# Performance work log

Hardware: AMD Instinct MI355X
Metric: run time of the kernel (lower is better)

The kernel has to match this reference:

```python
import jax, jax.numpy as jnp
import numpy as np

D_MODEL, H, D_FF = 1024, 16, 4096
D_K = D_MODEL // H
EPS = 1e-5


def _layernorm(x, alpha, bias):
    # faithful to source: unbiased std (ddof=1), eps added to std (not var)
    mean = jnp.mean(x, axis=-1, keepdims=True)
    std = jnp.std(x, axis=-1, keepdims=True, ddof=1)
    return alpha * (x - mean) / (std + EPS) + bias


def setup_inputs() -> dict:
    key = jax.random.key(0)
    ks = jax.random.split(key, 12)
    B, S = 2, 2048
    s = 1.0 / np.sqrt(D_MODEL)
    inp = {
        "x": jax.random.normal(ks[0], (B, S, D_MODEL), dtype=jnp.float32),
        "mask": jnp.ones((B, 1, 1, S), dtype=jnp.int32),
        "wq": jax.random.normal(ks[1], (D_MODEL, D_MODEL), dtype=jnp.float32) * s,
        "wk": jax.random.normal(ks[2], (D_MODEL, D_MODEL), dtype=jnp.float32) * s,
        "wv": jax.random.normal(ks[3], (D_MODEL, D_MODEL), dtype=jnp.float32) * s,
        "wo": jax.random.normal(ks[4], (D_MODEL, D_MODEL), dtype=jnp.float32) * s,
        "w1": jax.random.normal(ks[5], (D_MODEL, D_FF), dtype=jnp.float32) * s,
        "b1": jnp.zeros((D_FF,), dtype=jnp.float32),
        "w2": jax.random.normal(ks[6], (D_FF, D_MODEL), dtype=jnp.float32) * (1.0 / np.sqrt(D_FF)),
        "b2": jnp.zeros((D_MODEL,), dtype=jnp.float32),
        "alpha1": jnp.ones((1,), dtype=jnp.float32),
        "bias1": jnp.zeros((1,), dtype=jnp.float32),
        "alpha2": jnp.ones((1,), dtype=jnp.float32),
        "bias2": jnp.zeros((1,), dtype=jnp.float32),
    }
    return inp


def reference(x, mask, wq, wk, wv, wo, w1, b1, w2, b2, alpha1, bias1, alpha2, bias2):
    B, S, _ = x.shape

    # --- sublayer 1: pre-norm self-attention + residual ---
    xn = _layernorm(x, alpha1, bias1)
    q = (xn @ wq).reshape(B, S, H, D_K).transpose(0, 2, 1, 3)  # [B,H,S,Dk]
    k = (xn @ wk).reshape(B, S, H, D_K).transpose(0, 2, 1, 3)
    v = (xn @ wv).reshape(B, S, H, D_K).transpose(0, 2, 1, 3)

    scores = jnp.einsum("bhqd,bhkd->bhqk", q, k) / np.sqrt(D_K)  # [B,H,S,S]
    scores = jnp.where(mask == 0, jnp.float32(-1e9), scores)
    attn = jax.nn.softmax(scores, axis=-1)
    ctx = jnp.einsum("bhqk,bhkd->bhqd", attn, v)
    ctx = ctx.transpose(0, 2, 1, 3).reshape(B, S, D_MODEL)
    x = x + ctx @ wo

    # --- sublayer 2: pre-norm FFN + residual ---
    xn = _layernorm(x, alpha2, bias2)
    h = jax.nn.relu(xn @ w1 + b1)
    x = x + h @ w2 + b2
    return x
```

## Files before the change

kernel.cpp:

```cpp
#include <hip/hip_runtime.h>
#include <hip/hip_bf16.h>

typedef __attribute__((ext_vector_type(8))) short bf16x8;
typedef __attribute__((ext_vector_type(4))) short short4v;
typedef __attribute__((ext_vector_type(4))) float floatx4;

#define MFMA16(A, B, C) __builtin_amdgcn_mfma_f32_16x16x32_bf16((A), (B), (C), 0, 0, 0)

__device__ inline short bf16bits(float f) {
  __hip_bfloat16 h = __float2bfloat16(f);
  return *reinterpret_cast<short*>(&h);
}
__device__ inline unsigned cvtpk(float lo, float hi) {
  unsigned r;
  asm("v_cvt_pk_bf16_f32 %0, %1, %2" : "=v"(r) : "v"(lo), "v"(hi));
  return r;
}
typedef __attribute__((address_space(3))) char lds_char;
typedef __attribute__((address_space(1))) const char glob_char;
__device__ inline void gll16(const void* g, void* l) {
  __builtin_amdgcn_global_load_lds((glob_char*)g, (lds_char*)l, 16, 0, 0);
}

__global__ __launch_bounds__(256) void ln_qkvtrans_kernel(
    const float* __restrict__ x, __hip_bfloat16* __restrict__ y,
    const float* __restrict__ alpha_p, const float* __restrict__ bias_p,
    const float* __restrict__ wq, const float* __restrict__ wk,
    const float* __restrict__ wv, __hip_bfloat16* __restrict__ wqkvT) {
  __shared__ __align__(16) __hip_bfloat16 tile[64][72];
  const int bid = blockIdx.x;
  const int t = threadIdx.x;
  if (bid < 4096) {
    __shared__ float sred[8];
    const float* xr = x + (long)bid * 1024;
    float v[4];
#pragma unroll
    for (int i = 0; i < 4; i++) v[i] = xr[t * 4 + i];
    float sum = 0.f, sq = 0.f;
#pragma unroll
    for (int i = 0; i < 4; i++) { sum += v[i]; sq += v[i] * v[i]; }
#pragma unroll
    for (int off = 32; off; off >>= 1) {
      sum += __shfl_down(sum, off);
      sq += __shfl_down(sq, off);
    }
    if ((t & 63) == 0) { sred[(t >> 6) * 2] = sum; sred[(t >> 6) * 2 + 1] = sq; }
    __syncthreads();
    sum = sred[0] + sred[2] + sred[4] + sred[6];
    sq = sred[1] + sred[3] + sred[5] + sred[7];
    const float mean = sum * (1.f / 1024.f);
    float var = (sq - 1024.f * mean * mean) * (1.f / 1023.f);
    var = fmaxf(var, 0.f);
    const float denom = sqrtf(var) + 1e-5f;
    const float sc = alpha_p[0] / denom;
    const float beta = bias_p[0];
    __hip_bfloat16* yr = y + (long)bid * 1024;
#pragma unroll
    for (int i = 0; i < 4; i++) yr[t * 4 + i] = __float2bfloat16((v[i] - mean) * sc + beta);
  } else {
    const int tt = bid - 4096;
    const int which = tt >> 8;
    const float* src = which == 0 ? wq : (which == 1 ? wk : wv);
    __hip_bfloat16* dst = wqkvT + (size_t)which * 1024 * 1024;
    const long r0 = (long)((tt >> 4) & 15) * 64, c0 = (long)(tt & 15) * 64;
    for (int i = t; i < 1024; i += 256) {
      int r = i >> 4, c4 = (i & 15) * 4;
      float4 f = *(const float4*)&src[(r0 + r) * 1024 + c0 + c4];
      short4v s;
      s[0] = bf16bits(f.x); s[1] = bf16bits(f.y);
      s[2] = bf16bits(f.z); s[3] = bf16bits(f.w);
      *(short4v*)&tile[r][c4] = s;
    }
    __syncthreads();
    for (int i = t; i < 512; i += 256) {
      int c = i >> 3, r8 = (i & 7) * 8;
      bf16x8 sv;
#pragma unroll
      for (int j = 0; j < 8; j++) sv[j] = *reinterpret_cast<const short*>(&tile[r8 + j][c]);
      *(bf16x8*)&dst[(c0 + c) * 1024 + r0 + r8] = sv;
    }
  }
}

__global__ __launch_bounds__(256) void prep_kernel(
    const __hip_bfloat16* __restrict__ qkv, __hip_bfloat16* __restrict__ vt,
    const float* __restrict__ wo, __hip_bfloat16* __restrict__ woT,
    const int* __restrict__ mask, float* __restrict__ addm,
    int* __restrict__ flags) {
  __shared__ __align__(16) __hip_bfloat16 tile[64][72];
  __shared__ int ok[4];
  const int bid = blockIdx.x;
  if (bid < 1024) {
    const int bh = bid >> 5, b = bh >> 4, h = bh & 15;
    const long s0 = (long)(bid & 31) * 64;
    const __hip_bfloat16* src = qkv + ((long)b * 2048 + s0) * 3072 + 2048 + h * 64;
    for (int i = threadIdx.x; i < 512; i += 256) {
      int s = i >> 3, d8 = (i & 7) * 8;
      *(uint4*)&tile[s][d8] = *(const uint4*)&src[(long)s * 3072 + d8];
    }
    __syncthreads();
    __hip_bfloat16* dstb = vt + (long)bh * 64 * 2048 + s0;
    for (int i = threadIdx.x; i < 512; i += 256) {
      int d = i >> 3, s8 = (i & 7) * 8;
      bf16x8 sv;
#pragma unroll
      for (int j = 0; j < 8; j++) sv[j] = *reinterpret_cast<const short*>(&tile[s8 + j][d]);
      *(bf16x8*)&dstb[(long)d * 2048 + s8] = sv;
    }
  } else if (bid < 1280) {
    const int t = bid - 1024;
    const long r0 = (long)(t >> 4) * 64, c0 = (long)(t & 15) * 64;
    for (int i = threadIdx.x; i < 1024; i += 256) {
      int r = i >> 4, c4 = (i & 15) * 4;
      float4 f = *(const float4*)&wo[(r0 + r) * 1024 + c0 + c4];
      short4v s;
      s[0] = bf16bits(f.x); s[1] = bf16bits(f.y);
      s[2] = bf16bits(f.z); s[3] = bf16bits(f.w);
      *(short4v*)&tile[r][c4] = s;
    }
    __syncthreads();
    for (int i = threadIdx.x; i < 512; i += 256) {
      int c = i >> 3, r8 = (i & 7) * 8;
      bf16x8 sv;
#pragma unroll
      for (int j = 0; j < 8; j++) sv[j] = *reinterpret_cast<const short*>(&tile[r8 + j][c]);
      *(bf16x8*)&woT[(c0 + c) * 1024 + r0 + r8] = sv;
    }
  } else {
    const int i = (bid - 1280) * 256 + threadIdx.x;
    const int mv = mask[i];
    addm[i] = mv ? 0.f : -1e30f;
    const unsigned long long bal = __ballot(mv != 0);
    if ((threadIdx.x & 63) == 0) ok[threadIdx.x >> 6] = (bal == ~0ull) ? 1 : 0;
    __syncthreads();
    if (threadIdx.x == 0) flags[bid - 1280] = ok[0] & ok[1] & ok[2] & ok[3];
  }
}

__global__ __launch_bounds__(256) void ln2_wtrans_kernel(
    const float* __restrict__ x1, __hip_bfloat16* __restrict__ xn2,
    const float* __restrict__ alpha_p, const float* __restrict__ bias_p,
    const float* __restrict__ w1c, const float* __restrict__ w2c,
    __hip_bfloat16* __restrict__ w1Th, __hip_bfloat16* __restrict__ w2Th) {
  __shared__ __align__(16) __hip_bfloat16 tile[64][72];
  const int bid = blockIdx.x;
  const int t = threadIdx.x;
  if (bid < 4096) {
    __shared__ float sred[8];
    const float* xr = x1 + (long)bid * 1024;
    float v[4];
#pragma unroll
    for (int i = 0; i < 4; i++) v[i] = xr[t * 4 + i];
    float sum = 0.f, sq = 0.f;
#pragma unroll
    for (int i = 0; i < 4; i++) { sum += v[i]; sq += v[i] * v[i]; }
#pragma unroll
    for (int off = 32; off; off >>= 1) {
      sum += __shfl_down(sum, off);
      sq += __shfl_down(sq, off);
    }
    if ((t & 63) == 0) { sred[(t >> 6) * 2] = sum; sred[(t >> 6) * 2 + 1] = sq; }
    __syncthreads();
    sum = sred[0] + sred[2] + sred[4] + sred[6];
    sq = sred[1] + sred[3] + sred[5] + sred[7];
    const float mean = sum * (1.f / 1024.f);
    float var = (sq - 1024.f * mean * mean) * (1.f / 1023.f);
    var = fmaxf(var, 0.f);
    const float denom = sqrtf(var) + 1e-5f;
    const float sc = alpha_p[0] / denom;
    const float beta = bias_p[0];
    __hip_bfloat16* yr = xn2 + (long)bid * 1024;
#pragma unroll
    for (int i = 0; i < 4; i++) yr[t * 4 + i] = __float2bfloat16((v[i] - mean) * sc + beta);
  } else {
    const int wb = bid - 4096;
    const float* src;
    __hip_bfloat16* dst;
    int R, ldS;
    long r0, c0;
    if (wb < 512) {
      src = w1c; dst = w1Th; R = 1024; ldS = 4096;
      r0 = (long)(wb >> 5) * 64; c0 = (long)(wb & 31) * 64;
    } else {
      const int t2 = wb - 512;
      src = w2c; dst = w2Th; R = 2048; ldS = 1024;
      r0 = (long)(t2 >> 4) * 64; c0 = (long)(t2 & 15) * 64;
    }
    for (int i = t; i < 1024; i += 256) {
      int r = i >> 4, c4 = (i & 15) * 4;
      float4 f = *(const float4*)&src[(r0 + r) * ldS + c0 + c4];
      short4v s;
      s[0] = bf16bits(f.x); s[1] = bf16bits(f.y);
      s[2] = bf16bits(f.z); s[3] = bf16bits(f.w);
      *(short4v*)&tile[r][c4] = s;
    }
    __syncthreads();
    for (int i = t; i < 512; i += 256) {
      int c = i >> 3, r8 = (i & 7) * 8;
      bf16x8 sv;
#pragma unroll
      for (int j = 0; j < 8; j++) sv[j] = *reinterpret_cast<const short*>(&tile[r8 + j][c]);
      *(bf16x8*)&dst[(c0 + c) * R + r0 + r8] = sv;
    }
  }
}

__global__ __launch_bounds__(256) void wtrans_kernel(
    const float* __restrict__ w1c, const float* __restrict__ w2c,
    __hip_bfloat16* __restrict__ w1Th, __hip_bfloat16* __restrict__ w2Th) {
  __shared__ __align__(16) __hip_bfloat16 tile[64][72];
  const int bid = blockIdx.x;
  const float* src;
  __hip_bfloat16* dst;
  int R, ldS;
  long r0, c0;
  if (bid < 512) {
    src = w1c; dst = w1Th; R = 1024; ldS = 4096;
    r0 = (long)(bid >> 5) * 64; c0 = (long)(bid & 31) * 64;
  } else {
    const int t = bid - 512;
    src = w2c; dst = w2Th; R = 2048; ldS = 1024;
    r0 = (long)(t >> 4) * 64; c0 = (long)(t & 15) * 64;
  }
  for (int i = threadIdx.x; i < 1024; i += 256) {
    int r = i >> 4, c4 = (i & 15) * 4;
    float4 f = *(const float4*)&src[(r0 + r) * ldS + c0 + c4];
    short4v s;
    s[0] = bf16bits(f.x); s[1] = bf16bits(f.y);
    s[2] = bf16bits(f.z); s[3] = bf16bits(f.w);
    *(short4v*)&tile[r][c4] = s;
  }
  __syncthreads();
  for (int i = threadIdx.x; i < 512; i += 256) {
    int c = i >> 3, r8 = (i & 7) * 8;
    bf16x8 sv;
#pragma unroll
    for (int j = 0; j < 8; j++) sv[j] = *reinterpret_cast<const short*>(&tile[r8 + j][c]);
    *(bf16x8*)&dst[(c0 + c) * R + r0 + r8] = sv;
  }
}

__global__ __launch_bounds__(256) void bias_add_kernel(
    const float* __restrict__ x1, const float* __restrict__ b2,
    float* __restrict__ out) {
  const int i = (blockIdx.x * 256 + threadIdx.x) * 4;
  float4 v = *(const float4*)&x1[i];
  const float4 bb = *(const float4*)&b2[i & 1023];
  v.x += bb.x; v.y += bb.y; v.z += bb.z; v.w += bb.w;
  *(float4*)&out[i] = v;
}

template <int EPI>
__global__ __launch_bounds__(256) void gemm_bt_kernel(
    const __hip_bfloat16* __restrict__ A, const __hip_bfloat16* __restrict__ Bt,
    void* __restrict__ Cv, const float* __restrict__ bias,
    const float* __restrict__ res, int M, int N, int K) {
  __shared__ __align__(16) __hip_bfloat16 lA[2][128 * 32];
  __shared__ __align__(16) __hip_bfloat16 lB[2][128 * 32];
  const int tid = threadIdx.x;
  const int wave = tid >> 6, lane = tid & 63;
  const int quad = lane >> 4, l16 = lane & 15;
  const int wm = wave >> 1, wn = wave & 1;

  const int gx = gridDim.x;
  const int nwg = gx * gridDim.y;
  int bid = blockIdx.y * gx + blockIdx.x;
  bid = (bid & 7) * (nwg >> 3) + (bid >> 3);
  const long m0 = (long)(bid / gx) * 128;
  const long n0 = (long)(bid % gx) * 128;

  const int rA0 = tid >> 2, cA0 = (tid & 3) * 8;
  const int rA1 = (tid + 256) >> 2, cA1 = ((tid + 256) & 3) * 8;

  floatx4 acc[4][4];
#pragma unroll
  for (int i = 0; i < 4; i++)
#pragma unroll
    for (int j = 0; j < 4; j++) acc[i][j] = (floatx4){0.f, 0.f, 0.f, 0.f};

  const __hip_bfloat16* Ab = A + m0 * K;
  const __hip_bfloat16* Bb = Bt + n0 * K;

  gll16(&Ab[(long)rA0 * K + cA0], &lA[0][wave * 512]);
  gll16(&Ab[(long)rA1 * K + cA1], &lA[0][2048 + wave * 512]);
  gll16(&Bb[(long)rA0 * K + cA0], &lB[0][wave * 512]);
  gll16(&Bb[(long)rA1 * K + cA1], &lB[0][2048 + wave * 512]);

  int cur = 0;
  for (int k0 = 0; k0 < K; k0 += 32) {
    __syncthreads();
    if (k0 + 32 < K) {
      const int nxt = cur ^ 1;
      gll16(&Ab[(long)rA0 * K + k0 + 32 + cA0], &lA[nxt][wave * 512]);
      gll16(&Ab[(long)rA1 * K + k0 + 32 + cA1], &lA[nxt][2048 + wave * 512]);
      gll16(&Bb[(long)rA0 * K + k0 + 32 + cA0], &lB[nxt][wave * 512]);
      gll16(&Bb[(long)rA1 * K + k0 + 32 + cA1], &lB[nxt][2048 + wave * 512]);
    }
    bf16x8 af[4], bfr[4];
#pragma unroll
    for (int mi = 0; mi < 4; mi++)
      af[mi] = *(const bf16x8*)&lA[cur][(wm * 64 + mi * 16 + l16) * 32 + quad * 8];
#pragma unroll
    for (int ni = 0; ni < 4; ni++)
      bfr[ni] = *(const bf16x8*)&lB[cur][(wn * 64 + ni * 16 + l16) * 32 + quad * 8];
#pragma unroll
    for (int mi = 0; mi < 4; mi++)
#pragma unroll
      for (int ni = 0; ni < 4; ni++)
        acc[mi][ni] = MFMA16(af[mi], bfr[ni], acc[mi][ni]);
    cur ^= 1;
  }

#pragma unroll
  for (int mi = 0; mi < 4; mi++) {
#pragma unroll
    for (int ni = 0; ni < 4; ni++) {
#pragma unroll
      for (int r = 0; r < 4; r++) {
        const long row = m0 + wm * 64 + mi * 16 + quad * 4 + r;
        const long col = n0 + wn * 64 + ni * 16 + l16;
        const long idx = row * N + col;
        float v = acc[mi][ni][r];
        if (EPI == 0) {
          ((__hip_bfloat16*)Cv)[idx] = __float2bfloat16(v);
        } else if (EPI == 1) {
          ((float*)Cv)[idx] = v + res[idx];
        } else if (EPI == 2) {
          v += bias[col];
          ((__hip_bfloat16*)Cv)[idx] = __float2bfloat16(fmaxf(v, 0.f));
        } else if (EPI == 3) {
          float* Cf = (float*)Cv;
          Cf[idx] = Cf[idx] + v;
        }
      }
    }
  }
}

template <int EPI>
__global__ __launch_bounds__(256) void gemm_bt_k64_kernel(
    const __hip_bfloat16* __restrict__ A, const __hip_bfloat16* __restrict__ Bt,
    void* __restrict__ Cv, const float* __restrict__ bias,
    const float* __restrict__ res, int M, int N, int K) {
  __shared__ __align__(16) __hip_bfloat16 lA[2][128 * 64];
  __shared__ __align__(16) __hip_bfloat16 lB[2][128 * 64];
  const int tid = threadIdx.x;
  const int wave = tid >> 6, lane = tid & 63;
  const int quad = lane >> 4, l16 = lane & 15;
  const int wm = wave >> 1, wn = wave & 1;

  const int gx = gridDim.x;
  const int nwg = gx * gridDim.y;
  int bid = blockIdx.y * gx + blockIdx.x;
  bid = (bid & 7) * (nwg >> 3) + (bid >> 3);
  const long m0 = (long)(bid / gx) * 128;
  const long n0 = (long)(bid % gx) * 128;

  const int srow = lane >> 3;
  const int cg = (lane & 7) ^ srow;

  floatx4 acc[4][4];
#pragma unroll
  for (int i = 0; i < 4; i++)
#pragma unroll
    for (int j = 0; j < 4; j++) acc[i][j] = (floatx4){0.f, 0.f, 0.f, 0.f};

  const __hip_bfloat16* Ab = A + m0 * K;
  const __hip_bfloat16* Bb = Bt + n0 * K;

#pragma unroll
  for (int j = 0; j < 4; ++j) {
    const int c = wave + j * 4;
    gll16(&Ab[(long)(c * 8 + srow) * K + cg * 8], &lA[0][c * 512]);
    gll16(&Bb[(long)(c * 8 + srow) * K + cg * 8], &lB[0][c * 512]);
  }

  int cur = 0;
  for (int k0 = 0; k0 < K; k0 += 64) {
    __syncthreads();
    if (k0 + 64 < K) {
      const int nxt = cur ^ 1;
#pragma unroll
      for (int j = 0; j < 4; ++j) {
        const int c = wave + j * 4;
        gll16(&Ab[(long)(c * 8 + srow) * K + k0 + 64 + cg * 8], &lA[nxt][c * 512]);
        gll16(&Bb[(long)(c * 8 + srow) * K + k0 + 64 + cg * 8], &lB[nxt][c * 512]);
      }
    }
#pragma unroll
    for (int ks = 0; ks < 2; ++ks) {
      bf16x8 af[4], bfr[4];
#pragma unroll
      for (int mi = 0; mi < 4; mi++) {
        const int row = wm * 64 + mi * 16 + l16;
        af[mi] = *(const bf16x8*)&lA[cur][row * 64 +
                                          (((ks * 4 + quad) ^ (l16 & 7)) * 8)];
      }
#pragma unroll
      for (int ni = 0; ni < 4; ni++) {
        const int row = wn * 64 + ni * 16 + l16;
        bfr[ni] = *(const bf16x8*)&lB[cur][row * 64 +
                                           (((ks * 4 + quad) ^ (l16 & 7)) * 8)];
      }
#pragma unroll
      for (int mi = 0; mi < 4; mi++)
#pragma unroll
        for (int ni = 0; ni < 4; ni++)
          acc[mi][ni] = MFMA16(af[mi], bfr[ni], acc[mi][ni]);
    }
    cur ^= 1;
  }

#pragma unroll
  for (int mi = 0; mi < 4; mi++) {
#pragma unroll
    for (int ni = 0; ni < 4; ni++) {
#pragma unroll
      for (int r = 0; r < 4; r++) {
        const long row = m0 + wm * 64 + mi * 16 + quad * 4 + r;
        const long col = n0 + wn * 64 + ni * 16 + l16;
        const long idx = row * N + col;
        float v = acc[mi][ni][r];
        if (EPI == 0) {
          ((__hip_bfloat16*)Cv)[idx] = __float2bfloat16(v);
        } else if (EPI == 1) {
          ((float*)Cv)[idx] = v + res[idx];
        } else if (EPI == 2) {
          v += bias[col];
          ((__hip_bfloat16*)Cv)[idx] = __float2bfloat16(fmaxf(v, 0.f));
        } else if (EPI == 3) {
          float* Cf = (float*)Cv;
          Cf[idx] = Cf[idx] + v;
        }
      }
    }
  }
}

template <int EPI>
__global__ __launch_bounds__(256) void gemm64_bt_kernel(
    const __hip_bfloat16* __restrict__ A, const __hip_bfloat16* __restrict__ Bt,
    void* __restrict__ Cv, const float* __restrict__ bias,
    const float* __restrict__ res, int M, int N, int K) {
  __shared__ __align__(16) __hip_bfloat16 lA[2][128 * 64];
  __shared__ __align__(16) __hip_bfloat16 lB[2][64 * 64];
  const int tid = threadIdx.x;
  const int wave = tid >> 6, lane = tid & 63;
  const int quad = lane >> 4, l16 = lane & 15;
  const int wm = wave >> 1, wn = wave & 1;

  const int gx = gridDim.x;
  const int nwg = gx * gridDim.y;
  int bid = blockIdx.y * gx + blockIdx.x;
  bid = (bid & 7) * (nwg >> 3) + (bid >> 3);
  const long m0 = (long)(bid / gx) * 128;
  const long n0 = (long)(bid % gx) * 64;

  const int srow = lane >> 3;
  const int cg = (lane & 7) ^ srow;

  floatx4 acc[4][2];
#pragma unroll
  for (int i = 0; i < 4; i++)
#pragma unroll
    for (int j = 0; j < 2; j++) acc[i][j] = (floatx4){0.f, 0.f, 0.f, 0.f};

  const __hip_bfloat16* Ab = A + m0 * K;
  const __hip_bfloat16* Bb = Bt + n0 * K;

#pragma unroll
  for (int j = 0; j < 4; ++j) {
    const int c = wave + j * 4;
    gll16(&Ab[(long)(c * 8 + srow) * K + cg * 8], &lA[0][c * 512]);
  }
#pragma unroll
  for (int j = 0; j < 2; ++j) {
    const int c = wave + j * 4;
    gll16(&Bb[(long)(c * 8 + srow) * K + cg * 8], &lB[0][c * 512]);
  }

  int cur = 0;
  for (int k0 = 0; k0 < K; k0 += 64) {
    __syncthreads();
    if (k0 + 64 < K) {
      const int nxt = cur ^ 1;
#pragma unroll
      for (int j = 0; j < 4; ++j) {
        const int c = wave + j * 4;
        gll16(&Ab[(long)(c * 8 + srow) * K + k0 + 64 + cg * 8], &lA[nxt][c * 512]);
      }
#pragma unroll
      for (int j = 0; j < 2; ++j) {
        const int c = wave + j * 4;
        gll16(&Bb[(long)(c * 8 + srow) * K + k0 + 64 + cg * 8], &lB[nxt][c * 512]);
      }
    }
#pragma unroll
    for (int ks = 0; ks < 2; ++ks) {
      bf16x8 af[4], bfr[2];
#pragma unroll
      for (int mi = 0; mi < 4; mi++) {
        const int row = wm * 64 + mi * 16 + l16;
        af[mi] = *(const bf16x8*)&lA[cur][row * 64 +
                                          (((ks * 4 + quad) ^ (l16 & 7)) * 8)];
      }
#pragma unroll
      for (int ni = 0; ni < 2; ni++) {
        const int row = wn * 32 + ni * 16 + l16;
        bfr[ni] = *(const bf16x8*)&lB[cur][row * 64 +
                                           (((ks * 4 + quad) ^ (l16 & 7)) * 8)];
      }
#pragma unroll
      for (int mi = 0; mi < 4; mi++)
#pragma unroll
        for (int ni = 0; ni < 2; ni++)
          acc[mi][ni] = MFMA16(af[mi], bfr[ni], acc[mi][ni]);
    }
    cur ^= 1;
  }

#pragma unroll
  for (int mi = 0; mi < 4; mi++) {
#pragma unroll
    for (int ni = 0; ni < 2; ni++) {
#pragma unroll
      for (int r = 0; r < 4; r++) {
        const long row = m0 + wm * 64 + mi * 16 + quad * 4 + r;
        const long col = n0 + wn * 32 + ni * 16 + l16;
        const long idx = row * N + col;
        float v = acc[mi][ni][r];
        if (EPI == 1) {
          ((float*)Cv)[idx] = v + res[idx];
        } else if (EPI == 3) {
          float* Cf = (float*)Cv;
          Cf[idx] = Cf[idx] + v;
        }
      }
    }
  }
}

__global__ __launch_bounds__(256) void attn_kernel(
    const __hip_bfloat16* __restrict__ qkv, const __hip_bfloat16* __restrict__ vt,
    const float* __restrict__ addm, const int* __restrict__ flags,
    __hip_bfloat16* __restrict__ ctx) {
  __shared__ __align__(16) __hip_bfloat16 lK[2][64 * 64];
  __shared__ __align__(16) __hip_bfloat16 lV[2][64 * 64];
  __shared__ __align__(16) __hip_bfloat16 lP[4][16 * 64];
  const int tid = threadIdx.x, wave = tid >> 6, lane = tid & 63;
  const int quad = lane >> 4, l16 = lane & 15;
  const int nwg = gridDim.x * gridDim.y;
  int bid0 = blockIdx.y * gridDim.x + blockIdx.x;
  bid0 = (bid0 & 7) * (nwg >> 3) + (bid0 >> 3);
  const int bh = bid0 >> 5, b = bh >> 4, h = bh & 15;
  const int q0 = (bid0 & 31) * 64 + wave * 16;
  const float cs = 0.18033688011112042f;
  const float inv_cs = 5.545177444479562f;

  const __hip_bfloat16* kb = qkv + (long)b * 2048 * 3072 + 1024 + h * 64;
  const __hip_bfloat16* vb = vt + (long)bh * 64 * 2048;
  const float* am = addm + b * 2048;

  int fm = 1;
#pragma unroll
  for (int i = 0; i < 8; ++i) fm &= flags[b * 8 + i];
  const bool fast = (fm != 0);

  const long qoff = ((long)b * 2048 + q0 + l16) * 3072 + h * 64;
  const bf16x8 bq0 = *(const bf16x8*)&qkv[qoff + quad * 8];
  const bf16x8 bq1 = *(const bf16x8*)&qkv[qoff + 32 + quad * 8];

  const int srow = lane >> 3;
  const int cslot = lane & 7;
  const int cg = cslot ^ srow;
  const int rbase = wave * 16 + srow;

  char* const pbase = (char*)&lP[wave][0];
  const int prow = l16 * 128;
  const int pswz = l16 & 7;

  floatx4 o[4];
#pragma unroll
  for (int mi = 0; mi < 4; mi++) o[mi] = (floatx4){0.f, 0.f, 0.f, 0.f};
  float mrow = 10.0f, lrow = 0.f;

#pragma unroll
  for (int j = 0; j < 2; ++j) {
    const int rloc = rbase + j * 8;
    gll16(kb + (long)rloc * 3072 + cg * 8, &lK[0][(wave * 16 + j * 8) * 64]);
    gll16(vb + (long)rloc * 2048 + cg * 8, &lV[0][(wave * 16 + j * 8) * 64]);
  }

  int cur = 0;
  for (int t = 0; t < 32; ++t) {
    __syncthreads();
    if (t + 1 < 32) {
      const int nxt = cur ^ 1;
#pragma unroll
      for (int j = 0; j < 2; ++j) {
        const int rloc = rbase + j * 8;
        gll16(kb + (long)((t + 1) * 64 + rloc) * 3072 + cg * 8,
              &lK[nxt][(wave * 16 + j * 8) * 64]);
        gll16(vb + (long)rloc * 2048 + (t + 1) * 64 + cg * 8,
              &lV[nxt][(wave * 16 + j * 8) * 64]);
      }
    }
    const __hip_bfloat16* lKc = lK[cur];
    const __hip_bfloat16* lVc = lV[cur];

    floatx4 c[4];
    __builtin_amdgcn_s_setprio(1);
#pragma unroll
    for (int g = 0; g < 4; ++g) {
      const bf16x8 a0 =
          *(const bf16x8*)&lKc[(g * 16 + l16) * 64 + ((quad) ^ (l16 & 7)) * 8];
      const bf16x8 a1 =
          *(const bf16x8*)&lKc[(g * 16 + l16) * 64 + ((4 + quad) ^ (l16 & 7)) * 8];
      floatx4 cc = {0.f, 0.f, 0.f, 0.f};
      cc = MFMA16(a0, bq0, cc);
      cc = MFMA16(a1, bq1, cc);
      c[g] = cc;
    }
    __builtin_amdgcn_s_setprio(0);

    if (!fast) {
#pragma unroll
      for (int g = 0; g < 4; ++g) {
        const float4 a4 = *(const float4*)&am[t * 64 + g * 16 + quad * 4];
        c[g][0] = fmaf(a4.x, inv_cs, c[g][0]);
        c[g][1] = fmaf(a4.y, inv_cs, c[g][1]);
        c[g][2] = fmaf(a4.z, inv_cs, c[g][2]);
        c[g][3] = fmaf(a4.w, inv_cs, c[g][3]);
      }
    }

    const float mneg = -mrow;
    float p[4][4];
#pragma unroll
    for (int g = 0; g < 4; ++g)
#pragma unroll
      for (int r = 0; r < 4; ++r)
        p[g][r] = __builtin_amdgcn_exp2f(fmaf(c[g][r], cs, mneg));

#pragma unroll
    for (int g = 0; g < 4; ++g) {
      uint2 w2;
      w2.x = cvtpk(p[g][0], p[g][1]);
      w2.y = cvtpk(p[g][2], p[g][3]);
      const int slot16 = (g * 2 + (quad >> 1)) ^ pswz;
      *(uint2*)(pbase + prow + (slot16 << 4) + ((quad & 1) << 3)) = w2;
    }

    const float m0 = fmaxf(fmaxf(c[0][0], c[0][1]), c[0][2]);
    const float m1 = fmaxf(fmaxf(c[0][3], c[1][0]), c[1][1]);
    const float m2 = fmaxf(fmaxf(c[1][2], c[1][3]), c[2][0]);
    const float m3 = fmaxf(fmaxf(c[2][1], c[2][2]), c[2][3]);
    const float m4 = fmaxf(fmaxf(c[3][0], c[3][1]), c[3][2]);
    float tm = fmaxf(fmaxf(fmaxf(m0, m1), fmaxf(m2, m3)), fmaxf(m4, c[3][3]));
    tm = fmaxf(tm, __shfl_xor(tm, 16));
    tm = fmaxf(tm, __shfl_xor(tm, 32));
    const float tms = tm * cs;

    const float s0 = (p[0][0] + p[0][1]) + (p[0][2] + p[0][3]);
    const float s1 = (p[1][0] + p[1][1]) + (p[1][2] + p[1][3]);
    const float s2 = (p[2][0] + p[2][1]) + (p[2][2] + p[2][3]);
    const float s3 = (p[3][0] + p[3][1]) + (p[3][2] + p[3][3]);
    float rs = (s0 + s1) + (s2 + s3);
    rs += __shfl_xor(rs, 16);
    rs += __shfl_xor(rs, 32);

#pragma unroll
    for (int ss = 0; ss < 2; ++ss) {
      const bf16x8 bp = *(const bf16x8*)(pbase + prow +
                                         ((((ss << 2) + quad) ^ pswz) << 4));
      __builtin_amdgcn_s_setprio(1);
#pragma unroll
      for (int mi = 0; mi < 4; ++mi) {
        const bf16x8 av = *(const bf16x8*)&lVc[(mi * 16 + l16) * 64 +
                                               ((ss * 4 + quad) ^ (l16 & 7)) * 8];
        o[mi] = MFMA16(av, bp, o[mi]);
      }
      __builtin_amdgcn_s_setprio(0);
    }

    lrow += rs;
    if (__any(tms > mrow + 8.f)) {
      const float mnew = fmaxf(mrow, tms);
      const float alpha = __builtin_amdgcn_exp2f(mrow - mnew);
      mrow = mnew;
      lrow *= alpha;
#pragma unroll
      for (int mi = 0; mi < 4; mi++) o[mi] *= alpha;
    }
    cur ^= 1;
  }

  const float inv_l = 1.f / lrow;
  const long cb = ((long)b * 2048 + q0 + l16) * 1024 + h * 64;
#pragma unroll
  for (int mi = 0; mi < 4; mi++) {
    uint2 st;
    st.x = cvtpk(o[mi][0] * inv_l, o[mi][1] * inv_l);
    st.y = cvtpk(o[mi][2] * inv_l, o[mi][3] * inv_l);
    *(uint2*)&ctx[cb + mi * 16 + quad * 4] = st;
  }
}

extern "C" void kernel_launch(void* const* d_in, const int* in_sizes, int n_in,
                              void* d_out, int out_size, void* d_ws, size_t ws_size,
                              hipStream_t stream) {
  const float* x = (const float*)d_in[0];
  const int* mask = (const int*)d_in[1];
  const float* wq = (const float*)d_in[2];
  const float* wk = (const float*)d_in[3];
  const float* wv = (const float*)d_in[4];
  const float* wo = (const float*)d_in[5];
  const float* w1 = (const float*)d_in[6];
  const float* b1 = (const float*)d_in[7];
  const float* w2 = (const float*)d_in[8];
  const float* b2 = (const float*)d_in[9];
  const float* alpha1 = (const float*)d_in[10];
  const float* bias1 = (const float*)d_in[11];
  const float* alpha2 = (const float*)d_in[12];
  const float* bias2 = (const float*)d_in[13];

  char* ws = (char*)d_ws;
  char* dob = (char*)d_out;
  const size_t MiB = 1048576;
  __hip_bfloat16* qkv   = (__hip_bfloat16*)(ws + 0);
  __hip_bfloat16* wqkvT = (__hip_bfloat16*)(ws + 24 * MiB);
  __hip_bfloat16* vtb   = (__hip_bfloat16*)(ws + 24 * MiB);
  float*          x1    = (float*)(ws + 0);
  __hip_bfloat16* hc    = (__hip_bfloat16*)(ws + 16 * MiB);
  __hip_bfloat16* xn    = (__hip_bfloat16*)d_out;
  __hip_bfloat16* ctxb  = (__hip_bfloat16*)d_out;
  __hip_bfloat16* xn2   = (__hip_bfloat16*)d_out;
  __hip_bfloat16* woT   = (__hip_bfloat16*)(dob + 8 * MiB);
  __hip_bfloat16* w1Th  = (__hip_bfloat16*)(dob + 8 * MiB);
  __hip_bfloat16* w2Th  = (__hip_bfloat16*)(dob + 12 * MiB);
  float*          addm  = (float*)(dob + 12 * MiB);
  int*            flags = (int*)(dob + 12 * MiB + 16 * 1024);

  const dim3 b256(256);
  ln_qkvtrans_kernel<<<4864, b256, 0, stream>>>(x, xn, alpha1, bias1,
                                                wq, wk, wv, wqkvT);
  gemm_bt_kernel<0><<<dim3(24, 32), b256, 0, stream>>>(xn, wqkvT, qkv, nullptr,
                                                       nullptr, 4096, 3072, 1024);
  prep_kernel<<<1296, b256, 0, stream>>>(qkv, vtb, wo, woT, mask, addm, flags);
  attn_kernel<<<dim3(32, 32), b256, 0, stream>>>(qkv, vtb, addm, flags, ctxb);
  gemm64_bt_kernel<1><<<dim3(16, 32), b256, 0, stream>>>(ctxb, woT, x1, nullptr, x,
                                                         4096, 1024, 1024);
  ln2_wtrans_kernel<<<5120, b256, 0, stream>>>(x1, xn2, alpha2, bias2,
                                               w1, w2, w1Th, w2Th);
  gemm_bt_k64_kernel<2><<<dim3(16, 32), b256, 0, stream>>>(xn2, w1Th, hc,
                                                           b1, nullptr,
                                                           4096, 2048, 1024);
  gemm64_bt_kernel<3><<<dim3(16, 32), b256, 0, stream>>>(hc, w2Th, x1, nullptr,
                                                         nullptr, 4096, 1024, 2048);
  wtrans_kernel<<<1024, b256, 0, stream>>>(w1 + 2048,
                                           w2 + (size_t)2048 * 1024,
                                           w1Th, w2Th);
  gemm_bt_k64_kernel<2><<<dim3(16, 32), b256, 0, stream>>>(xn2, w1Th, hc,
                                                           b1 + 2048, nullptr,
                                                           4096, 2048, 1024);
  gemm64_bt_kernel<3><<<dim3(16, 32), b256, 0, stream>>>(hc, w2Th, x1, nullptr,
                                                         nullptr, 4096, 1024, 2048);
  bias_add_kernel<<<4096, b256, 0, stream>>>(x1, b2, (float*)d_out);
}
```

Baseline: 383.6 us.

## Software-pipeline attention PV matmul one tile behind and use wave-per-row layernorm

The attention loop now issues the P·V MFMAs for the previous key tile before the QK^T and softmax of the current tile. V gets a triple-buffered LDS ring so the lagging tile stays valid while the next one loads, and the goal is to overlap MFMA work with the exp/reduction latency. Separately, both layernorm paths switch to one wave per row with float4 loads, xor-shuffle reductions, and packed bf16 stores. This drops the block-level LDS reduction and barrier and uses 4x fewer blocks. The extra V buffer raises LDS usage and may reduce occupancy.

```diff
diff --git a/kernel.cpp b/kernel.cpp
--- a/kernel.cpp
+++ b/kernel.cpp
@@ -30,35 +30,41 @@
   __shared__ __align__(16) __hip_bfloat16 tile[64][72];
   const int bid = blockIdx.x;
   const int t = threadIdx.x;
-  if (bid < 4096) {
-    __shared__ float sred[8];
-    const float* xr = x + (long)bid * 1024;
-    float v[4];
-#pragma unroll
-    for (int i = 0; i < 4; i++) v[i] = xr[t * 4 + i];
+  if (bid < 1024) {
+    const int wvv = t >> 6, lane = t & 63;
+    const long row = (long)bid * 4 + wvv;
+    const float* xr = x + row * 1024;
+    float4 v4[4];
+#pragma unroll
+    for (int i = 0; i < 4; i++) v4[i] = *(const float4*)&xr[lane * 4 + i * 256];
     float sum = 0.f, sq = 0.f;
 #pragma unroll
-    for (int i = 0; i < 4; i++) { sum += v[i]; sq += v[i] * v[i]; }
+    for (int i = 0; i < 4; i++) {
+      sum += (v4[i].x + v4[i].y) + (v4[i].z + v4[i].w);
+      sq += (v4[i].x * v4[i].x + v4[i].y * v4[i].y) +
+            (v4[i].z * v4[i].z + v4[i].w * v4[i].w);
+    }
 #pragma unroll
     for (int off = 32; off; off >>= 1) {
-      sum += __shfl_down(sum, off);
-      sq += __shfl_down(sq, off);
-    }
-    if ((t & 63) == 0) { sred[(t >> 6) * 2] = sum; sred[(t >> 6) * 2 + 1] = sq; }
-    __syncthreads();
-    sum = sred[0] + sred[2] + sred[4] + sred[6];
-    sq = sred[1] + sred[3] + sred[5] + sred[7];
+      sum += __shfl_xor(sum, off);
+      sq += __shfl_xor(sq, off);
+    }
     const float mean = sum * (1.f / 1024.f);
     float var = (sq - 1024.f * mean * mean) * (1.f / 1023.f);
     var = fmaxf(var, 0.f);
     const float denom = sqrtf(var) + 1e-5f;
     const float sc = alpha_p[0] / denom;
     const float beta = bias_p[0];
-    __hip_bfloat16* yr = y + (long)bid * 1024;
-#pragma unroll
-    for (int i = 0; i < 4; i++) yr[t * 4 + i] = __float2bfloat16((v[i] - mean) * sc + beta);
+    __hip_bfloat16* yr = y + row * 1024;
+#pragma unroll
+    for (int i = 0; i < 4; i++) {
+      uint2 st;
+      st.x = cvtpk((v4[i].x - mean) * sc + beta, (v4[i].y - mean) * sc + beta);
+      st.y = cvtpk((v4[i].z - mean) * sc + beta, (v4[i].w - mean) * sc + beta);
+      *(uint2*)&yr[lane * 4 + i * 256] = st;
+    }
   } else {
-    const int tt = bid - 4096;
+    const int tt = bid - 1024;
     const int which = tt >> 8;
     const float* src = which == 0 ? wq : (which == 1 ? wk : wv);
     __hip_bfloat16* dst = wqkvT + (size_t)which * 1024 * 1024;
@@ -145,35 +151,41 @@
   __shared__ __align__(16) __hip_bfloat16 tile[64][72];
   const int bid = blockIdx.x;
   const int t = threadIdx.x;
-  if (bid < 4096) {
-    __shared__ float sred[8];
-    const float* xr = x1 + (long)bid * 1024;
-    float v[4];
-#pragma unroll
-    for (int i = 0; i < 4; i++) v[i] = xr[t * 4 + i];
+  if (bid < 1024) {
+    const int wvv = t >> 6, lane = t & 63;
+    const long row = (long)bid * 4 + wvv;
+    const float* xr = x1 + row * 1024;
+    float4 v4[4];
+#pragma unroll
+    for (int i = 0; i < 4; i++) v4[i] = *(const float4*)&xr[lane * 4 + i * 256];
     float sum = 0.f, sq = 0.f;
 #pragma unroll
-    for (int i = 0; i < 4; i++) { sum += v[i]; sq += v[i] * v[i]; }
+    for (int i = 0; i < 4; i++) {
+      sum += (v4[i].x + v4[i].y) + (v4[i].z + v4[i].w);
+      sq += (v4[i].x * v4[i].x + v4[i].y * v4[i].y) +
+            (v4[i].z * v4[i].z + v4[i].w * v4[i].w);
+    }
 #pragma unroll
     for (int off = 32; off; off >>= 1) {
-      sum += __shfl_down(sum, off);
-      sq += __shfl_down(sq, off);
-    }
-    if ((t & 63) == 0) { sred[(t >> 6) * 2] = sum; sred[(t >> 6) * 2 + 1] = sq; }
-    __syncthreads();
-    sum = sred[0] + sred[2] + sred[4] + sred[6];
-    sq = sred[1] + sred[3] + sred[5] + sred[7];
+      sum += __shfl_xor(sum, off);
+      sq += __shfl_xor(sq, off);
+    }
     const float mean = sum * (1.f / 1024.f);
     float var = (sq - 1024.f * mean * mean) * (1.f / 1023.f);
     var = fmaxf(var, 0.f);
     const float denom = sqrtf(var) + 1e-5f;
     const float sc = alpha_p[0] / denom;
     const float beta = bias_p[0];
-    __hip_bfloat16* yr = xn2 + (long)bid * 1024;
-#pragma unroll
-    for (int i = 0; i < 4; i++) yr[t * 4 + i] = __float2bfloat16((v[i] - mean) * sc + beta);
+    __hip_bfloat16* yr = xn2 + row * 1024;
+#pragma unroll
+    for (int i = 0; i < 4; i++) {
+      uint2 st;
+      st.x = cvtpk((v4[i].x - mean) * sc + beta, (v4[i].y - mean) * sc + beta);
+      st.y = cvtpk((v4[i].z - mean) * sc + beta, (v4[i].w - mean) * sc + beta);
+      *(uint2*)&yr[lane * 4 + i * 256] = st;
+    }
   } else {
-    const int wb = bid - 4096;
+    const int wb = bid - 1024;
     const float* src;
     __hip_bfloat16* dst;
     int R, ldS;
@@ -545,7 +557,7 @@
     const float* __restrict__ addm, const int* __restrict__ flags,
     __hip_bfloat16* __restrict__ ctx) {
   __shared__ __align__(16) __hip_bfloat16 lK[2][64 * 64];
-  __shared__ __align__(16) __hip_bfloat16 lV[2][64 * 64];
+  __shared__ __align__(16) __hip_bfloat16 lV[3][64 * 64];
   __shared__ __align__(16) __hip_bfloat16 lP[4][16 * 64];
   const int tid = threadIdx.x, wave = tid >> 6, lane = tid & 63;
   const int quad = lane >> 4, l16 = lane & 15;
@@ -583,6 +595,7 @@
 #pragma unroll
   for (int mi = 0; mi < 4; mi++) o[mi] = (floatx4){0.f, 0.f, 0.f, 0.f};
   float mrow = 10.0f, lrow = 0.f;
+  float rs_prev = 0.f, tms_prev = -3.0e38f;
 
 #pragma unroll
   for (int j = 0; j < 2; ++j) {
@@ -591,108 +604,117 @@
     gll16(vb + (long)rloc * 2048 + cg * 8, &lV[0][(wave * 16 + j * 8) * 64]);
   }
 
-  int cur = 0;
-  for (int t = 0; t < 32; ++t) {
+  int kcur = 0;
+  int vN = 1;
+  int vP = 2;
+  for (int t = 0; t <= 32; ++t) {
     __syncthreads();
     if (t + 1 < 32) {
-      const int nxt = cur ^ 1;
+      const int knxt = kcur ^ 1;
 #pragma unroll
       for (int j = 0; j < 2; ++j) {
         const int rloc = rbase + j * 8;
         gll16(kb + (long)((t + 1) * 64 + rloc) * 3072 + cg * 8,
-              &lK[nxt][(wave * 16 + j * 8) * 64]);
+              &lK[knxt][(wave * 16 + j * 8) * 64]);
         gll16(vb + (long)rloc * 2048 + (t + 1) * 64 + cg * 8,
-              &lV[nxt][(wave * 16 + j * 8) * 64]);
-      }
-    }
-    const __hip_bfloat16* lKc = lK[cur];
-    const __hip_bfloat16* lVc = lV[cur];
-
-    floatx4 c[4];
-    __builtin_amdgcn_s_setprio(1);
-#pragma unroll
-    for (int g = 0; g < 4; ++g) {
-      const bf16x8 a0 =
-          *(const bf16x8*)&lKc[(g * 16 + l16) * 64 + ((quad) ^ (l16 & 7)) * 8];
-      const bf16x8 a1 =
-          *(const bf16x8*)&lKc[(g * 16 + l16) * 64 + ((4 + quad) ^ (l16 & 7)) * 8];
-      floatx4 cc = {0.f, 0.f, 0.f, 0.f};
-      cc = MFMA16(a0, bq0, cc);
-      cc = MFMA16(a1, bq1, cc);
-      c[g] = cc;
-    }
-    __builtin_amdgcn_s_setprio(0);
-
-    if (!fast) {
+              &lV[vN][(wave * 16 + j * 8) * 64]);
+      }
+    }
+
+    if (t >= 1) {
+      const __hip_bfloat16* lVp = lV[vP];
+#pragma unroll
+      for (int ss = 0; ss < 2; ++ss) {
+        const bf16x8 bp = *(const bf16x8*)(pbase + prow +
+                                           ((((ss << 2) + quad) ^ pswz) << 4));
+        __builtin_amdgcn_s_setprio(1);
+#pragma unroll
+        for (int mi = 0; mi < 4; ++mi) {
+          const bf16x8 av = *(const bf16x8*)&lVp[(mi * 16 + l16) * 64 +
+                                                 ((ss * 4 + quad) ^ (l16 & 7)) * 8];
+          o[mi] = MFMA16(av, bp, o[mi]);
+        }
+        __builtin_amdgcn_s_setprio(0);
+      }
+      lrow += rs_prev;
+      if (__any(tms_prev > mrow + 8.f)) {
+        const float mnew = fmaxf(mrow, tms_prev);
+        const float alpha = __builtin_amdgcn_exp2f(mrow - mnew);
+        mrow = mnew;
+        lrow *= alpha;
+#pragma unroll
+        for (int mi = 0; mi < 4; mi++) o[mi] *= alpha;
+      }
+    }
+
+    if (t < 32) {
+      const __hip_bfloat16* lKc = lK[kcur];
+      floatx4 c[4];
+      __builtin_amdgcn_s_setprio(1);
 #pragma unroll
       for (int g = 0; g < 4; ++g) {
-        const float4 a4 = *(const float4*)&am[t * 64 + g * 16 + quad * 4];
-        c[g][0] = fmaf(a4.x, inv_cs, c[g][0]);
-        c[g][1] = fmaf(a4.y, inv_cs, c[g][1]);
-        c[g][2] = fmaf(a4.z, inv_cs, c[g][2]);
-        c[g][3] = fmaf(a4.w, inv_cs, c[g][3]);
-      }
-    }
-
-    const float mneg = -mrow;
-    float p[4][4];
-#pragma unroll
-    for (int g = 0; g < 4; ++g)
-#pragma unroll
-      for (int r = 0; r < 4; ++r)
-        p[g][r] = __builtin_amdgcn_exp2f(fmaf(c[g][r], cs, mneg));
-
-#pragma unroll
-    for (int g = 0; g < 4; ++g) {
-      uint2 w2;
-      w2.x = cvtpk(p[g][0], p[g][1]);
-      w2.y = cvtpk(p[g][2], p[g][3]);
-      const int slot16 = (g * 2 + (quad >> 1)) ^ pswz;
-      *(uint2*)(pbase + prow + (slot16 << 4) + ((quad & 1) << 3)) = w2;
-    }
-
-    const float m0 = fmaxf(fmaxf(c[0][0], c[0][1]), c[0][2]);
-    const float m1 = fmaxf(fmaxf(c[0][3], c[1][0]), c[1][1]);
-    const float m2 = fmaxf(fmaxf(c[1][2], c[1][3]), c[2][0]);
-    const float m3 = fmaxf(fmaxf(c[2][1], c[2][2]), c[2][3]);
-    const float m4 = fmaxf(fmaxf(c[3][0], c[3][1]), c[3][2]);
-    float tm = fmaxf(fmaxf(fmaxf(m0, m1), fmaxf(m2, m3)), fmaxf(m4, c[3][3]));
-    tm = fmaxf(tm, __shfl_xor(tm, 16));
-    tm = fmaxf(tm, __shfl_xor(tm, 32));
-    const float tms = tm * cs;
-
-    const float s0 = (p[0][0] + p[0][1]) + (p[0][2] + p[0][3]);
-    const float s1 = (p[1][0] + p[1][1]) + (p[1][2] + p[1][3]);
-    const float s2 = (p[2][0] + p[2][1]) + (p[2][2] + p[2][3]);
-    const float s3 = (p[3][0] + p[3][1]) + (p[3][2] + p[3][3]);
-    float rs = (s0 + s1) + (s2 + s3);
-    rs += __shfl_xor(rs, 16);
-    rs += __shfl_xor(rs, 32);
-
-#pragma unroll
-    for (int ss = 0; ss < 2; ++ss) {
-      const bf16x8 bp = *(const bf16x8*)(pbase + prow +
-                                         ((((ss << 2) + quad) ^ pswz) << 4));
-      __builtin_amdgcn_s_setprio(1);
-#pragma unroll
-      for (int mi = 0; mi < 4; ++mi) {
-        const bf16x8 av = *(const bf16x8*)&lVc[(mi * 16 + l16) * 64 +
-                                               ((ss * 4 + quad) ^ (l16 & 7)) * 8];
-        o[mi] = MFMA16(av, bp, o[mi]);
+        const bf16x8 a0 =
+            *(const bf16x8*)&lKc[(g * 16 + l16) * 64 + ((quad) ^ (l16 & 7)) * 8];
+        const bf16x8 a1 =
+            *(const bf16x8*)&lKc[(g * 16 + l16) * 64 + ((4 + quad) ^ (l16 & 7)) * 8];
+        floatx4 cc = {0.f, 0.f, 0.f, 0.f};
+        cc = MFMA16(a0, bq0, cc);
+        cc = MFMA16(a1, bq1, cc);
+        c[g] = cc;
       }
       __builtin_amdgcn_s_setprio(0);
-    }
-
-    lrow += rs;
-    if (__any(tms > mrow + 8.f)) {
-      const float mnew = fmaxf(mrow, tms);
-      const float alpha = __builtin_amdgcn_exp2f(mrow - mnew);
-      mrow = mnew;
-      lrow *= alpha;
-#pragma unroll
-      for (int mi = 0; mi < 4; mi++) o[mi] *= alpha;
-    }
-    cur ^= 1;
+
+      if (!fast) {
+#pragma unroll
+        for (int g = 0; g < 4; ++g) {
+          const float4 a4 = *(const float4*)&am[t * 64 + g * 16 + quad * 4];
+          c[g][0] = fmaf(a4.x, inv_cs, c[g][0]);
+          c[g][1] = fmaf(a4.y, inv_cs, c[g][1]);
+          c[g][2] = fmaf(a4.z, inv_cs, c[g][2]);
+          c[g][3] = fmaf(a4.w, inv_cs, c[g][3]);
+        }
+      }
+
+      const float mneg = -mrow;
+      float p[4][4];
+#pragma unroll
+      for (int g = 0; g < 4; ++g)
+#pragma unroll
+        for (int r = 0; r < 4; ++r)
+          p[g][r] = __builtin_amdgcn_exp2f(fmaf(c[g][r], cs, mneg));
+
+#pragma unroll
+      for (int g = 0; g < 4; ++g) {
+        uint2 w2;
+        w2.x = cvtpk(p[g][0], p[g][1]);
+        w2.y = cvtpk(p[g][2], p[g][3]);
+        const int slot16 = (g * 2 + (quad >> 1)) ^ pswz;
+        *(uint2*)(pbase + prow + (slot16 << 4) + ((quad & 1) << 3)) = w2;
+      }
+
+      const float m0 = fmaxf(fmaxf(c[0][0], c[0][1]), c[0][2]);
+      const float m1 = fmaxf(fmaxf(c[0][3], c[1][0]), c[1][1]);
+      const float m2 = fmaxf(fmaxf(c[1][2], c[1][3]), c[2][0]);
+      const float m3 = fmaxf(fmaxf(c[2][1], c[2][2]), c[2][3]);
+      const float m4 = fmaxf(fmaxf(c[3][0], c[3][1]), c[3][2]);
+      float tm = fmaxf(fmaxf(fmaxf(m0, m1), fmaxf(m2, m3)), fmaxf(m4, c[3][3]));
+      tm = fmaxf(tm, __shfl_xor(tm, 16));
+      tm = fmaxf(tm, __shfl_xor(tm, 32));
+      tms_prev = tm * cs;
+
+      const float s0 = (p[0][0] + p[0][1]) + (p[0][2] + p[0][3]);
+      const float s1 = (p[1][0] + p[1][1]) + (p[1][2] + p[1][3]);
+      const float s2 = (p[2][0] + p[2][1]) + (p[2][2] + p[2][3]);
+      const float s3 = (p[3][0] + p[3][1]) + (p[3][2] + p[3][3]);
+      float rs = (s0 + s1) + (s2 + s3);
+      rs += __shfl_xor(rs, 16);
+      rs += __shfl_xor(rs, 32);
+      rs_prev = rs;
+    }
+
+    kcur ^= 1;
+    vN = (vN == 2) ? 0 : vN + 1;
+    vP = (vP == 2) ? 0 : vP + 1;
   }
 
   const float inv_l = 1.f / lrow;
@@ -742,7 +764,7 @@
   int*            flags = (int*)(dob + 12 * MiB + 16 * 1024);
 
   const dim3 b256(256);
-  ln_qkvtrans_kernel<<<4864, b256, 0, stream>>>(x, xn, alpha1, bias1,
+  ln_qkvtrans_kernel<<<1792, b256, 0, stream>>>(x, xn, alpha1, bias1,
                                                 wq, wk, wv, wqkvT);
   gemm_bt_kernel<0><<<dim3(24, 32), b256, 0, stream>>>(xn, wqkvT, qkv, nullptr,
                                                        nullptr, 4096, 3072, 1024);
@@ -750,7 +772,7 @@
   attn_kernel<<<dim3(32, 32), b256, 0, stream>>>(qkv, vtb, addm, flags, ctxb);
   gemm64_bt_kernel<1><<<dim3(16, 32), b256, 0, stream>>>(ctxb, woT, x1, nullptr, x,
                                                          4096, 1024, 1024);
-  ln2_wtrans_kernel<<<5120, b256, 0, stream>>>(x1, xn2, alpha2, bias2,
+  ln2_wtrans_kernel<<<2048, b256, 0, stream>>>(x1, xn2, alpha2, bias2,
                                                w1, w2, w1Th, w2Th);
   gemm_bt_k64_kernel<2><<<dim3(16, 32), b256, 0, stream>>>(xn2, w1Th, hc,
                                                            b1, nullptr,
```

Result: slower. 401.4 us (+4.7%).
